# Kernel tuning notes

Measured on AMD Instinct MI355X. Metric: run time of the kernel, lower is better.

## Reference

```python
import jax, jax.numpy as jnp
import numpy as np
import math

D_MODEL = 1024
N_HEADS = 16
D_HEAD = D_MODEL // N_HEADS
NUM_BUCKETS = 32
MAX_DISTANCE = 128
B, LQ, LK = 2, 2048, 2048


def _rel_pos_bucket(rel):
    # rel: [Lq, Lk] int32, rel = mem - ctx
    n = jnp.clip(-rel, 0, None)
    max_exact = NUM_BUCKETS // 2
    is_small = n < max_exact
    val_if_large = max_exact + (
        jnp.log(n.astype(jnp.float32) / max_exact + 1e-9)
        / math.log(MAX_DISTANCE / max_exact)
        * (NUM_BUCKETS - max_exact)
    ).astype(jnp.int32)
    val_if_large = jnp.minimum(val_if_large, NUM_BUCKETS - 1)
    return jnp.where(is_small, n, val_if_large)


def setup_inputs() -> dict:
    key = jax.random.key(0)
    ks = jax.random.split(key, 9)
    scale = 1.0 / math.sqrt(D_MODEL)
    q = jax.random.normal(ks[0], (B, LQ, D_MODEL), dtype=jnp.float32)
    k = jax.random.normal(ks[1], (B, LK, D_MODEL), dtype=jnp.float32)
    v = jax.random.normal(ks[2], (B, LK, D_MODEL), dtype=jnp.float32)
    key_padding_mask = jax.random.randint(ks[3], (B, 1, 1, LK), 0, 2).astype(bool)
    Wq = jax.random.normal(ks[4], (D_MODEL, D_MODEL), dtype=jnp.float32) * scale
    Wk = jax.random.normal(ks[5], (D_MODEL, D_MODEL), dtype=jnp.float32) * scale
    Wv = jax.random.normal(ks[6], (D_MODEL, D_MODEL), dtype=jnp.float32) * scale
    Wo = jax.random.normal(ks[7], (D_MODEL, D_MODEL), dtype=jnp.float32) * scale
    rel_emb = jax.random.normal(ks[8], (NUM_BUCKETS, N_HEADS), dtype=jnp.float32) * 0.02
    return {"q": q, "k": k, "v": v, "key_padding_mask": key_padding_mask,
            "Wq": Wq, "Wk": Wk, "Wv": Wv, "Wo": Wo, "rel_emb": rel_emb}


def reference(q, k, v, key_padding_mask, Wq, Wk, Wv, Wo, rel_emb):
    Bq, Lq, _ = q.shape
    Lk = k.shape[1]
    # projections (nn.Linear: x @ W.T), split heads -> [B, H, L, dh]
    qh = (q @ Wq.T).reshape(Bq, Lq, N_HEADS, D_HEAD).transpose(0, 2, 1, 3)
    kh = (k @ Wk.T).reshape(Bq, Lk, N_HEADS, D_HEAD).transpose(0, 2, 1, 3)
    vh = (v @ Wv.T).reshape(Bq, Lk, N_HEADS, D_HEAD).transpose(0, 2, 1, 3)
    scores = jnp.einsum('bhqd,bhkd->bhqk', qh, kh) / math.sqrt(D_HEAD)
    # relative position bias: [1, H, Lq, Lk]
    rel = jnp.arange(Lk, dtype=jnp.int32)[None, :] - jnp.arange(Lq, dtype=jnp.int32)[:, None]
    buckets = _rel_pos_bucket(rel)  # [Lq, Lk]
    bias = rel_emb[buckets]         # [Lq, Lk, H]
    scores = scores + bias.transpose(2, 0, 1)[None]
    scores = jnp.where(key_padding_mask, scores, -1e9)
    attn = jax.nn.softmax(scores, axis=-1)
    out = jnp.einsum('bhqk,bhkd->bhqd', attn, vh)
    out = out.transpose(0, 2, 1, 3).reshape(Bq, Lq, D_MODEL)
    return out @ Wo.T
```

## Files before the change

kernel.cpp:

```cpp
#include <hip/hip_runtime.h>
#include <math.h>

typedef _Float16 f16;
typedef __fp16 h16x2 __attribute__((ext_vector_type(2)));
typedef _Float16 f16x4 __attribute__((ext_vector_type(4)));
typedef _Float16 f16x8 __attribute__((ext_vector_type(8)));
typedef float f32x4 __attribute__((ext_vector_type(4)));
typedef float f32x16 __attribute__((ext_vector_type(16)));
typedef unsigned int u32;

#define D_MODEL 1024
#define NHEADS 16
#define DHEAD 64
#define LQ 2048
#define LKK 2048
#define BB 2
#define LOG2E 1.4426950408889634f

static __device__ __forceinline__ void gload16(const void* g, void* l) {
  __builtin_amdgcn_global_load_lds(
      (const __attribute__((address_space(1))) u32*)g,
      (__attribute__((address_space(3))) u32*)l, 16, 0, 0);
}
static __device__ __forceinline__ float ex2(float x) {
  float r;
  asm volatile("v_exp_f32 %0, %1\n\ts_nop 0" : "=v"(r) : "v"(x));
  return r;
}
static __device__ __forceinline__ u32 pkr(float a, float b) {
  union { h16x2 h; u32 u; } c;
  c.h = __builtin_amdgcn_cvt_pkrtz(a, b);
  return c.u;
}
static __device__ __forceinline__ float fmax3(float a, float b, float c) {
  return fmaxf(fmaxf(a, b), c);
}
#define MFMA16(a, b, c) __builtin_amdgcn_mfma_f32_16x16x32_f16(a, b, c, 0, 0, 0)
#define MFMA32(a, b, c) __builtin_amdgcn_mfma_f32_32x32x16_f16(a, b, c, 0, 0, 0)

__global__ void k_prep(const void* msk, const float* __restrict__ rel,
                       float* __restrict__ biasT, unsigned char* __restrict__ m8) {
  __shared__ int o1s, o2s;
  const int t = threadIdx.x;
  if (t == 0) { o1s = 0; o2s = 0; }
  __syncthreads();
  const unsigned char* raw = (const unsigned char*)msk;
  int o1 = 0, o2 = 0;
  for (int i = t; i < BB * LKK; i += 256) {
    unsigned char vv = raw[i];
    if ((i & 3) && vv) o1 = 1;
    if (((i & 3) == 2) && vv == 0x80u) o2 = 1;
  }
  if (o1) atomicOr(&o1s, 1);
  if (o2) atomicOr(&o2s, 1);
  __syncthreads();
  const int f = o1s ? (o2s ? 2 : 1) : 0;
  for (int i = t; i < BB * LKK; i += 256) {
    unsigned char v;
    if (f == 0)      v = (((const int*)msk)[i] != 0);
    else if (f == 1) v = (((const unsigned char*)msk)[i] != 0);
    else             v = (((const float*)msk)[i] != 0.0f);
    m8[i] = v;
  }
  for (int n = t; n < 2048; n += 256) {
    int bucket;
    if (n < 16) bucket = n;
    else {
      float tt = logf((float)n / 16.0f + 1e-9f);
      tt = tt / 2.0794415416798357f;
      tt = tt * 16.0f;
      bucket = 16 + (int)tt;
      if (bucket > 31) bucket = 31;
    }
    for (int h = 0; h < NHEADS; ++h)
      biasT[h * 2048 + n] = rel[bucket * NHEADS + h] * LOG2E;
  }
}

__global__ void k_cvt_all(const float* q, const float* k, const float* v,
                          const float* Wq, const float* Wk, const float* Wv, const float* Wo,
                          f16* Xq, f16* Xk, f16* Xv, f16* W16) {
  int i = blockIdx.x * 256 + threadIdx.x;
  const float* s; f16* d; int off;
  if (i < 3145728) {
    int which = i >> 20; off = i & 1048575;
    s = which == 0 ? q : (which == 1 ? k : v);
    d = which == 0 ? Xq : (which == 1 ? Xk : Xv);
  } else {
    int j = i - 3145728; int which = j >> 18; off = j & 262143;
    s = which == 0 ? Wq : (which == 1 ? Wk : (which == 2 ? Wv : Wo));
    d = W16 + which * 1048576;
  }
  float4 x = ((const float4*)s)[off];
  f16x4 o; o[0] = (f16)x.x; o[1] = (f16)x.y; o[2] = (f16)x.z; o[3] = (f16)x.w;
  ((f16x4*)d)[off] = o;
}

template <int EPI>
static __device__ __forceinline__ void gemm_core(const f16* __restrict__ A,
                                                 const f16* __restrict__ Bm,
                                                 void* __restrict__ C) {
  __shared__ __align__(16) f16 sA[128 * 32];
  __shared__ __align__(16) f16 sB[128 * 32];
  const int t = threadIdx.x;
  const int w = t >> 6, lane = t & 63;
  const int lg = lane >> 4, lc = lane & 15;
  const int wr = w >> 1, wc = w & 1;
  const long row0 = (long)blockIdx.x * 128;
  const long col0 = (long)blockIdx.y * 128;
  f32x4 acc[4][4] = {};

  for (int kk = 0; kk < 1024; kk += 32) {
#pragma unroll
    for (int it = 0; it < 2; ++it) {
      int ch = t + it * 256;
      int r = ch >> 2, kg = ch & 3;
      gload16(A + (row0 + r) * 1024 + kk + kg * 8, (char*)sA + ch * 16);
      gload16(Bm + (col0 + r) * 1024 + kk + kg * 8, (char*)sB + ch * 16);
    }
    __syncthreads();
    f16x8 af[4], bf[4];
#pragma unroll
    for (int i = 0; i < 4; ++i)
      af[i] = *(const f16x8*)&sA[(wr * 64 + i * 16 + lc) * 32 + lg * 8];
#pragma unroll
    for (int j = 0; j < 4; ++j)
      bf[j] = *(const f16x8*)&sB[(wc * 64 + j * 16 + lc) * 32 + lg * 8];
#pragma unroll
    for (int i = 0; i < 4; ++i)
#pragma unroll
      for (int j = 0; j < 4; ++j)
        acc[i][j] = MFMA16(af[i], bf[j], acc[i][j]);
    __syncthreads();
  }
#pragma unroll
  for (int i = 0; i < 4; ++i)
#pragma unroll
    for (int j = 0; j < 4; ++j) {
      const long rowb = row0 + wr * 64 + i * 16 + lg * 4;
      const long col = col0 + wc * 64 + j * 16 + lc;
      if (EPI == 2) {
        long b = rowb >> 11, l0 = rowb & 2047;
        long h = col >> 6, d = col & 63;
        f16x4 ov;
#pragma unroll
        for (int r = 0; r < 4; ++r) ov[r] = (f16)acc[i][j][r];
        *(f16x4*)((f16*)C + (((b * NHEADS + h) * DHEAD + d) * (long)LKK + l0)) = ov;
      } else {
#pragma unroll
        for (int r = 0; r < 4; ++r) {
          long row = rowb + r;
          float v = acc[i][j][r];
          if (EPI == 0) {
            long b = row >> 11, l = row & 2047;
            long h = col >> 6, d = col & 63;
            ((f16*)C)[(((b * NHEADS + h) * LQ) + l) * DHEAD + d] = (f16)v;
          } else {
            ((float*)C)[row * 1024 + col] = v;
          }
        }
      }
    }
}

__global__ void __launch_bounds__(256, 3)
k_gemm_qkv(const f16* __restrict__ Xq, const f16* __restrict__ Xk, const f16* __restrict__ Xv,
           const f16* __restrict__ W16, f16* __restrict__ QHp, f16* __restrict__ KHp,
           f16* __restrict__ VTp, int zoff) {
  const int z = blockIdx.z + zoff;
  if (z == 2) {
    gemm_core<2>(Xv, W16 + 2 * 1048576, VTp);
  } else {
    const f16* A = z == 0 ? Xq : Xk;
    const f16* Bm = W16 + (size_t)z * 1048576;
    f16* C = z == 0 ? QHp : KHp;
    gemm_core<0>(A, Bm, C);
  }
}

__global__ void __launch_bounds__(256, 2)
k_gemm_o(const f16* __restrict__ A, const f16* __restrict__ Bm, float* __restrict__ C) {
  gemm_core<1>(A, Bm, C);
}

__global__ void __launch_bounds__(256, 2)
k_attn(const f16* __restrict__ QH, const f16* __restrict__ KH, const f16* __restrict__ VT,
       const float* __restrict__ BIASg, const unsigned char* __restrict__ M8,
       f16* __restrict__ O16) {
  __shared__ __align__(16) f16 sK[2][64 * 64];
  __shared__ __align__(16) f16 sVT[2][64 * 64];
  __shared__ __align__(16) float sBias[4104];
  __shared__ __align__(16) float sPen[2048];

  const int L = blockIdx.x;
  const int bh = (L & 7) * 4 + ((L >> 3) & 3);
  const int qc = L >> 5;
  const int b = bh >> 4, h = bh & 15;
  const int t = threadIdx.x, w = t >> 6, lane = t & 63;
  const int lq = lane & 31;
  const int hi = lane >> 5;
  const int q0w = qc * 128 + w * 32;
  const size_t base = (size_t)bh * LKK * DHEAD;

  for (int i = t; i < 4104; i += 256) {
    int n = i - 2052; n = n < 0 ? 0 : (n > 2047 ? 2047 : n);
    sBias[i] = BIASg[h * 2048 + n];
  }
  for (int i = t; i < 2048; i += 256)
    sPen[i] = M8[b * LKK + i] ? 0.0f : -3.0e9f;

  f16x8 qb[4];
  const f16* qrow = QH + base + (size_t)(q0w + lq) * DHEAD;
#pragma unroll
  for (int s = 0; s < 4; ++s)
    qb[s] = *(const f16x8*)(qrow + s * 16 + hi * 8);

  const int ch0 = t, ch1 = t + 256;
  const int r0 = ch0 >> 3, g0 = ((ch0 & 7) ^ (r0 & 7)) * 8;
  const int r1 = ch1 >> 3, g1 = ((ch1 & 7) ^ (r1 & 7)) * 8;
  const f16* Kb = KH + base;
  const f16* Vb = VT + base;

  auto STAGE = [&](int kt, int buf) {
    const int k0 = kt * 64;
    gload16(Kb + (size_t)(k0 + r0) * DHEAD + g0, (char*)&sK[buf][0] + ch0 * 16);
    gload16(Kb + (size_t)(k0 + r1) * DHEAD + g1, (char*)&sK[buf][0] + ch1 * 16);
    gload16(Vb + (size_t)r0 * LKK + k0 + g0, (char*)&sVT[buf][0] + ch0 * 16);
    gload16(Vb + (size_t)r1 * LKK + k0 + g1, (char*)&sVT[buf][0] + ch1 * 16);
  };

  float m_r = -1e30f;
  f32x16 oacc0 = {}, oacc1 = {}, oaccL = {};
  const float c1 = 0.125f * LOG2E;
  f16x8 ones;
#pragma unroll
  for (int e = 0; e < 8; ++e) ones[e] = (f16)1.0f;

  STAGE(0, 0);
  __syncthreads();

  for (int kt = 0; kt < 32; ++kt) {
    const int cur = kt & 1;
    if (kt < 31) STAGE(kt + 1, cur ^ 1);

    f32x16 sa0 = {}, sa1 = {};
#pragma unroll
    for (int s = 0; s < 4; ++s) {
      f16x8 k0 = *(const f16x8*)((const char*)&sK[cur][0] +
                   ((lq * 128 + s * 32 + hi * 16) ^ ((lq & 7) << 4)));
      f16x8 k1 = *(const f16x8*)((const char*)&sK[cur][0] +
                   (((32 + lq) * 128 + s * 32 + hi * 16) ^ ((lq & 7) << 4)));
      sa0 = MFMA32(k0, qb[s], sa0);
      sa1 = MFMA32(k1, qb[s], sa1);
    }

    float p_[32];
#pragma unroll
    for (int r = 0; r < 16; ++r) { p_[r] = sa0[r]; p_[16 + r] = sa1[r]; }

#pragma unroll
    for (int u = 0; u < 8; ++u) {
      int tt = u >> 2, j = u & 3;
      int kbase = kt * 64 + tt * 32 + j * 8 + hi * 4;
      f32x4 pen4 = *(const f32x4*)&sPen[kbase];
      int bidx0 = (q0w + lq) - kbase + 2052;
#pragma unroll
      for (int e = 0; e < 4; ++e) {
        float bp = sBias[bidx0 - e] + pen4[e];
        int r = tt * 16 + j * 4 + e;
        p_[r] = p_[r] * c1 + bp;
      }
    }

    float mm[11];
#pragma unroll
    for (int r = 0; r < 10; ++r) mm[r] = fmax3(p_[3 * r], p_[3 * r + 1], p_[3 * r + 2]);
    mm[10] = fmaxf(p_[30], p_[31]);
    float a0 = fmax3(mm[0], mm[1], mm[2]);
    float a1 = fmax3(mm[3], mm[4], mm[5]);
    float a2 = fmax3(mm[6], mm[7], mm[8]);
    float a3 = fmax3(mm[9], mm[10], a0);
    float mx = fmax3(a1, a2, a3);
    mx = fmaxf(mx, __shfl_xor(mx, 32));

    if (__any(mx > m_r + 8.0f)) {
      float mnew = fmaxf(m_r, mx);
      float al = ex2(m_r - mnew);
      m_r = mnew;
#pragma unroll
      for (int r = 0; r < 16; ++r) { oacc0[r] *= al; oacc1[r] *= al; oaccL[r] *= al; }
    }

#pragma unroll
    for (int r = 0; r < 32; ++r) p_[r] = ex2(p_[r] - m_r);

    f16x8 pf[4];
#pragma unroll
    for (int sl = 0; sl < 4; ++sl) {
      int tt = sl >> 1, sp = sl & 1;
      int bA = tt * 16 + (2 * sp) * 4, bB = tt * 16 + (2 * sp + 1) * 4;
      u32 A0 = pkr(p_[bA], p_[bA + 1]);
      u32 A1 = pkr(p_[bA + 2], p_[bA + 3]);
      u32 B0 = pkr(p_[bB], p_[bB + 1]);
      u32 B1 = pkr(p_[bB + 2], p_[bB + 3]);
      asm volatile("v_permlane32_swap_b32 %0, %1" : "+v"(A0), "+v"(B0));
      asm volatile("v_permlane32_swap_b32 %0, %1" : "+v"(A1), "+v"(B1));
      union { u32 u[4]; f16x8 v; } c;
      c.u[0] = A0; c.u[1] = A1; c.u[2] = B0; c.u[3] = B1;
      pf[sl] = c.v;
    }

#pragma unroll
    for (int sl = 0; sl < 4; ++sl) {
      int K0 = sl * 16;
      f16x8 v0 = *(const f16x8*)((const char*)&sVT[cur][0] +
                   ((lq * 128 + K0 * 2 + hi * 16) ^ ((lq & 7) << 4)));
      f16x8 v1 = *(const f16x8*)((const char*)&sVT[cur][0] +
                   (((32 + lq) * 128 + K0 * 2 + hi * 16) ^ ((lq & 7) << 4)));
      oacc0 = MFMA32(v0, pf[sl], oacc0);
      oacc1 = MFMA32(v1, pf[sl], oacc1);
      oaccL = MFMA32(ones, pf[sl], oaccL);
    }
    __syncthreads();
  }

  const float rinv = 1.0f / oaccL[0];
  const size_t orow = ((size_t)b * LQ + (q0w + lq)) * D_MODEL + h * DHEAD;
#pragma unroll
  for (int dh = 0; dh < 2; ++dh)
#pragma unroll
    for (int j = 0; j < 4; ++j) {
      int d0 = dh * 32 + j * 8 + hi * 4;
      f16x4 ov;
#pragma unroll
      for (int e = 0; e < 4; ++e) {
        float x = (dh ? oacc1[j * 4 + e] : oacc0[j * 4 + e]) * rinv;
        ov[e] = (f16)x;
      }
      *(f16x4*)(O16 + orow + d0) = ov;
    }
}

extern "C" void kernel_launch(void* const* d_in, const int* in_sizes, int n_in,
                              void* d_out, int out_size, void* d_ws, size_t ws_size,
                              hipStream_t stream) {
  (void)in_sizes; (void)n_in; (void)out_size;
  const float* q   = (const float*)d_in[0];
  const float* k   = (const float*)d_in[1];
  const float* v   = (const float*)d_in[2];
  const void*  msk = d_in[3];
  const float* Wq  = (const float*)d_in[4];
  const float* Wk  = (const float*)d_in[5];
  const float* Wv  = (const float*)d_in[6];
  const float* Wo  = (const float*)d_in[7];
  const float* rel = (const float*)d_in[8];

  char* ws = (char*)d_ws;
  const size_t SL = (size_t)8 << 20;
  const bool bigA = ws_size >= 8 * SL;

  f16 *Xq, *Xk, *Xv, *QHp, *KHp, *VTp, *O16, *W16; char* misc;
  if (bigA) {
    Xq = (f16*)(ws + 0 * SL); Xk = (f16*)(ws + 1 * SL); Xv = (f16*)(ws + 2 * SL);
    QHp = (f16*)(ws + 3 * SL); KHp = (f16*)(ws + 4 * SL); VTp = (f16*)(ws + 5 * SL);
    W16 = (f16*)(ws + 6 * SL); O16 = (f16*)(ws + 2 * SL);
    misc = ws + 7 * SL;
  } else {
    Xq = (f16*)(ws + 0 * SL); Xk = (f16*)(ws + 1 * SL); Xv = (f16*)(ws + 2 * SL);
    QHp = (f16*)(ws + 3 * SL); KHp = (f16*)(ws + 0 * SL); VTp = (f16*)(ws + 1 * SL);
    W16 = (f16*)(ws + 4 * SL); O16 = (f16*)(ws + 2 * SL);
    misc = ws + 5 * SL;
  }
  float* BIAS = (float*)misc;
  unsigned char* M8 = (unsigned char*)(misc + (192 << 10));

  k_prep<<<1, 256, 0, stream>>>(msk, rel, BIAS, M8);
  k_cvt_all<<<16384, 256, 0, stream>>>(q, k, v, Wq, Wk, Wv, Wo, Xq, Xk, Xv, W16);

  if (bigA) {
    k_gemm_qkv<<<dim3(32, 8, 3), 256, 0, stream>>>(Xq, Xk, Xv, W16, QHp, KHp, VTp, 0);
  } else {
    for (int z = 0; z < 3; ++z)
      k_gemm_qkv<<<dim3(32, 8, 1), 256, 0, stream>>>(Xq, Xk, Xv, W16, QHp, KHp, VTp, z);
  }
  k_attn<<<512, 256, 0, stream>>>(QHp, KHp, VTp, BIAS, M8, O16);
  k_gemm_o<<<dim3(32, 8), 256, 0, stream>>>(O16, W16 + 3 * 1048576, (float*)d_out);
}
```

Measured before the change: 155.1 us.

## Software-pipeline attention QK with softmax/PV and narrow output GEMM tiles

The attention loop now stages K and V separately and computes the QK scores of the next key tile while softmax and PV run on the current one, using two score register sets. `s_setprio` raises wave priority around the MFMA sections. The output projection GEMM switches to 128x64 tiles, launching twice as many blocks to fill more CUs. The extra live score registers add register pressure. The first K-tile refill can be issued before other waves have finished reading that buffer, which is a possible race.

Result: no change. 152.2 us (-1.9%).

```diff
diff --git a/kernel.cpp b/kernel.cpp
--- a/kernel.cpp
+++ b/kernel.cpp
@@ -96,19 +96,20 @@
   ((f16x4*)d)[off] = o;
 }
 
-template <int EPI>
+template <int EPI, int BN>
 static __device__ __forceinline__ void gemm_core(const f16* __restrict__ A,
                                                  const f16* __restrict__ Bm,
                                                  void* __restrict__ C) {
+  constexpr int JN = BN / 32;
   __shared__ __align__(16) f16 sA[128 * 32];
-  __shared__ __align__(16) f16 sB[128 * 32];
+  __shared__ __align__(16) f16 sB[BN * 32];
   const int t = threadIdx.x;
   const int w = t >> 6, lane = t & 63;
   const int lg = lane >> 4, lc = lane & 15;
   const int wr = w >> 1, wc = w & 1;
   const long row0 = (long)blockIdx.x * 128;
-  const long col0 = (long)blockIdx.y * 128;
-  f32x4 acc[4][4] = {};
+  const long col0 = (long)blockIdx.y * BN;
+  f32x4 acc[4][JN] = {};
 
   for (int kk = 0; kk < 1024; kk += 32) {
 #pragma unroll
@@ -116,29 +117,34 @@
       int ch = t + it * 256;
       int r = ch >> 2, kg = ch & 3;
       gload16(A + (row0 + r) * 1024 + kk + kg * 8, (char*)sA + ch * 16);
+    }
+#pragma unroll
+    for (int it = 0; it < BN / 64; ++it) {
+      int ch = t + it * 256;
+      int r = ch >> 2, kg = ch & 3;
       gload16(Bm + (col0 + r) * 1024 + kk + kg * 8, (char*)sB + ch * 16);
     }
     __syncthreads();
-    f16x8 af[4], bf[4];
+    f16x8 af[4], bf[JN];
 #pragma unroll
     for (int i = 0; i < 4; ++i)
       af[i] = *(const f16x8*)&sA[(wr * 64 + i * 16 + lc) * 32 + lg * 8];
 #pragma unroll
-    for (int j = 0; j < 4; ++j)
-      bf[j] = *(const f16x8*)&sB[(wc * 64 + j * 16 + lc) * 32 + lg * 8];
+    for (int j = 0; j < JN; ++j)
+      bf[j] = *(const f16x8*)&sB[(wc * (16 * JN) + j * 16 + lc) * 32 + lg * 8];
 #pragma unroll
     for (int i = 0; i < 4; ++i)
 #pragma unroll
-      for (int j = 0; j < 4; ++j)
+      for (int j = 0; j < JN; ++j)
         acc[i][j] = MFMA16(af[i], bf[j], acc[i][j]);
     __syncthreads();
   }
 #pragma unroll
   for (int i = 0; i < 4; ++i)
 #pragma unroll
-    for (int j = 0; j < 4; ++j) {
+    for (int j = 0; j < JN; ++j) {
       const long rowb = row0 + wr * 64 + i * 16 + lg * 4;
-      const long col = col0 + wc * 64 + j * 16 + lc;
+      const long col = col0 + wc * (16 * JN) + j * 16 + lc;
       if (EPI == 2) {
         long b = rowb >> 11, l0 = rowb & 2047;
         long h = col >> 6, d = col & 63;
@@ -169,18 +175,18 @@
            f16* __restrict__ VTp, int zoff) {
   const int z = blockIdx.z + zoff;
   if (z == 2) {
-    gemm_core<2>(Xv, W16 + 2 * 1048576, VTp);
+    gemm_core<2, 128>(Xv, W16 + 2 * 1048576, VTp);
   } else {
     const f16* A = z == 0 ? Xq : Xk;
     const f16* Bm = W16 + (size_t)z * 1048576;
     f16* C = z == 0 ? QHp : KHp;
-    gemm_core<0>(A, Bm, C);
+    gemm_core<0, 128>(A, Bm, C);
   }
 }
 
 __global__ void __launch_bounds__(256, 2)
 k_gemm_o(const f16* __restrict__ A, const f16* __restrict__ Bm, float* __restrict__ C) {
-  gemm_core<1>(A, Bm, C);
+  gemm_core<1, 64>(A, Bm, C);
 }
 
 __global__ void __launch_bounds__(256, 2)
@@ -221,10 +227,13 @@
   const f16* Kb = KH + base;
   const f16* Vb = VT + base;
 
-  auto STAGE = [&](int kt, int buf) {
+  auto STAGE_K = [&](int kt, int buf) {
     const int k0 = kt * 64;
     gload16(Kb + (size_t)(k0 + r0) * DHEAD + g0, (char*)&sK[buf][0] + ch0 * 16);
     gload16(Kb + (size_t)(k0 + r1) * DHEAD + g1, (char*)&sK[buf][0] + ch1 * 16);
+  };
+  auto STAGE_V = [&](int kt, int buf) {
+    const int k0 = kt * 64;
     gload16(Vb + (size_t)r0 * LKK + k0 + g0, (char*)&sVT[buf][0] + ch0 * 16);
     gload16(Vb + (size_t)r1 * LKK + k0 + g1, (char*)&sVT[buf][0] + ch1 * 16);
   };
@@ -236,24 +245,20 @@
 #pragma unroll
   for (int e = 0; e < 8; ++e) ones[e] = (f16)1.0f;
 
-  STAGE(0, 0);
-  __syncthreads();
-
-  for (int kt = 0; kt < 32; ++kt) {
-    const int cur = kt & 1;
-    if (kt < 31) STAGE(kt + 1, cur ^ 1);
-
-    f32x16 sa0 = {}, sa1 = {};
+  auto QK = [&](int kt, f32x16& sa0, f32x16& sa1) {
+    const char* sKb = (const char*)&sK[kt & 1][0];
+    __builtin_amdgcn_s_setprio(1);
 #pragma unroll
     for (int s = 0; s < 4; ++s) {
-      f16x8 k0 = *(const f16x8*)((const char*)&sK[cur][0] +
-                   ((lq * 128 + s * 32 + hi * 16) ^ ((lq & 7) << 4)));
-      f16x8 k1 = *(const f16x8*)((const char*)&sK[cur][0] +
-                   (((32 + lq) * 128 + s * 32 + hi * 16) ^ ((lq & 7) << 4)));
+      f16x8 k0 = *(const f16x8*)(sKb + ((lq * 128 + s * 32 + hi * 16) ^ ((lq & 7) << 4)));
+      f16x8 k1 = *(const f16x8*)(sKb + (((32 + lq) * 128 + s * 32 + hi * 16) ^ ((lq & 7) << 4)));
       sa0 = MFMA32(k0, qb[s], sa0);
       sa1 = MFMA32(k1, qb[s], sa1);
     }
-
+    __builtin_amdgcn_s_setprio(0);
+  };
+
+  auto SOFTPV = [&](int kt, f32x16& sa0, f32x16& sa1) {
     float p_[32];
 #pragma unroll
     for (int r = 0; r < 16; ++r) { p_[r] = sa0[r]; p_[16 + r] = sa1[r]; }
@@ -310,17 +315,41 @@
       pf[sl] = c.v;
     }
 
+    const char* sVb = (const char*)&sVT[kt & 1][0];
+    __builtin_amdgcn_s_setprio(1);
 #pragma unroll
     for (int sl = 0; sl < 4; ++sl) {
       int K0 = sl * 16;
-      f16x8 v0 = *(const f16x8*)((const char*)&sVT[cur][0] +
-                   ((lq * 128 + K0 * 2 + hi * 16) ^ ((lq & 7) << 4)));
-      f16x8 v1 = *(const f16x8*)((const char*)&sVT[cur][0] +
-                   (((32 + lq) * 128 + K0 * 2 + hi * 16) ^ ((lq & 7) << 4)));
+      f16x8 v0 = *(const f16x8*)(sVb + ((lq * 128 + K0 * 2 + hi * 16) ^ ((lq & 7) << 4)));
+      f16x8 v1 = *(const f16x8*)(sVb + (((32 + lq) * 128 + K0 * 2 + hi * 16) ^ ((lq & 7) << 4)));
       oacc0 = MFMA32(v0, pf[sl], oacc0);
       oacc1 = MFMA32(v1, pf[sl], oacc1);
       oaccL = MFMA32(ones, pf[sl], oaccL);
     }
+    __builtin_amdgcn_s_setprio(0);
+  };
+
+  STAGE_K(0, 0);
+  STAGE_V(0, 0);
+  STAGE_K(1, 1);
+  __syncthreads();
+  f32x16 sA0 = {}, sA1 = {}, sB0 = {}, sB1 = {};
+  QK(0, sA0, sA1);
+
+  for (int kt = 0; kt < 32; kt += 2) {
+    if (kt + 2 < 32) STAGE_K(kt + 2, 0);
+    STAGE_V(kt + 1, 1);
+    sB0 = f32x16{}; sB1 = f32x16{};
+    QK(kt + 1, sB0, sB1);
+    SOFTPV(kt, sA0, sA1);
+    __syncthreads();
+    if (kt + 3 < 32) STAGE_K(kt + 3, 1);
+    if (kt + 2 < 32) {
+      STAGE_V(kt + 2, 0);
+      sA0 = f32x16{}; sA1 = f32x16{};
+      QK(kt + 2, sA0, sA1);
+    }
+    SOFTPV(kt + 1, sB0, sB1);
     __syncthreads();
   }
 
@@ -384,5 +413,5 @@
       k_gemm_qkv<<<dim3(32, 8, 1), 256, 0, stream>>>(Xq, Xk, Xv, W16, QHp, KHp, VTp, z);
   }
   k_attn<<<512, 256, 0, stream>>>(QHp, KHp, VTp, BIAS, M8, O16);
-  k_gemm_o<<<dim3(32, 8), 256, 0, stream>>>(O16, W16 + 3 * 1048576, (float*)d_out);
-}
+  k_gemm_o<<<dim3(32, 16), 256, 0, stream>>>(O16, W16 + 3 * 1048576, (float*)d_out);
+}
```
